# Kernel optimization log

Hardware: AMD Instinct MI355X
Metric: run time of the kernel (lower is better)

The kernel has to match this reference:

```python
import jax, jax.numpy as jnp
import numpy as np
from jax import lax

S, T, B = 32, 32, 512          # src len, tgt len, batch
H, E, A = 1024, 256, 1024      # hidden, embed, attention dim
VS, VT = 64, 70                # source / target char vocab
START = 1                      # data.tar_l2i[start_token]


def _gru_cell(gi, h, W_hh, b_hh):
    """torch GRUCell math. gi = x @ W_ih.T + b_ih, shape (B, 3H)."""
    gh = h @ W_hh.T + b_hh
    ir, iz, in_ = jnp.split(gi, 3, axis=-1)
    hr, hz, hn = jnp.split(gh, 3, axis=-1)
    r = jax.nn.sigmoid(ir + hr)
    z = jax.nn.sigmoid(iz + hz)
    n = jnp.tanh(in_ + r * hn)
    return (1.0 - z) * n + z * h


def setup_inputs() -> dict:
    key = jax.random.key(0)
    ks = jax.random.split(key, 16)
    n = lambda k, shp: jax.random.normal(k, shp, dtype=jnp.float32) * 0.05
    return {
        "source": jax.random.randint(ks[0], (S, B), 0, VS),
        "target": jax.random.randint(ks[1], (T, B), 0, VT),
        "teacher_forcing": 1,
        "emb_src": n(ks[2], (VS, E)),
        "W_ih_enc": n(ks[3], (3 * H, E)),
        "W_hh_enc": n(ks[4], (3 * H, H)),
        "b_ih_enc": n(ks[5], (3 * H,)),
        "b_hh_enc": n(ks[6], (3 * H,)),
        "emb_tgt": n(ks[7], (VT, E)),
        "W_attn": n(ks[8], (2 * H, A)),
        "b_attn": n(ks[9], (A,)),
        "v_attn": n(ks[10], (A,)),
        "W_ih_dec": n(ks[11], (3 * H, H + E)),
        "W_hh_dec": n(ks[12], (3 * H, H)),
        "b_ih_dec": n(ks[13], (3 * H,)),
        "b_hh_dec": n(ks[14], (3 * H,)),
        "W_out": n(ks[15], (H, VT)),
        "b_out": jnp.zeros((VT,), jnp.float32),
    }


def reference(source, target, teacher_forcing, emb_src, W_ih_enc, W_hh_enc,
              b_ih_enc, b_hh_enc, emb_tgt, W_attn, b_attn, v_attn,
              W_ih_dec, W_hh_dec, b_ih_dec, b_hh_dec, W_out, b_out):
    tf = bool(teacher_forcing)

    # ---------------- Encoder: GRU over (S, B) ----------------
    x_emb = emb_src[source]                                   # (S, B, E)
    # precompute input-to-hidden GEMM for all timesteps (big fused GEMM)
    gi_all = jnp.einsum('sbe,ge->sbg', x_emb, W_ih_enc) + b_ih_enc  # (S, B, 3H)

    def enc_step(h, gi_t):
        h = _gru_cell(gi_t, h, W_hh_enc, b_hh_enc)
        return h, h

    h0 = jnp.zeros((B, H), x_emb.dtype)
    h_enc, enc_ops = lax.scan(enc_step, h0, gi_all)           # enc_ops: (S, B, H)

    # ---------------- Decoder loop (t = 1 .. T-1) ----------------
    def dec_step(carry, tgt_t):
        h, x = carry
        emb = emb_tgt[x]                                      # (B, E)
        hx = jnp.broadcast_to(h[None], (S, B, H))
        feat = jnp.concatenate([hx, enc_ops], axis=-1)        # (S, B, 2H)
        energy = jnp.tanh(jnp.einsum('sbf,fa->sba', feat, W_attn) + b_attn)
        scores = energy @ v_attn                              # (S, B)
        alpha = jax.nn.softmax(scores, axis=0)                # over source positions
        ctx = jnp.einsum('sb,sbh->bh', alpha, enc_ops)        # (B, H)
        gi = jnp.concatenate([ctx, emb], axis=-1) @ W_ih_dec.T + b_ih_dec
        h_new = _gru_cell(gi, h, W_hh_dec, b_hh_dec)
        logits = h_new @ W_out + b_out                        # (B, VT)
        x_next = tgt_t if tf else jnp.argmax(logits, axis=1)
        return (h_new, x_next), (logits, alpha.T)             # attn row: (B, S)

    (_, _), (dec_logits, attn) = lax.scan(dec_step, (h_enc, target[0]), target[1:])

    # outputs[0] is the one-hot start token (outputs[:, :, start]=1, rows 1.. overwritten)
    row0 = jnp.zeros((B, VT), dec_logits.dtype).at[:, START].set(1.0)
    outputs = jnp.concatenate([row0[None], dec_logits], axis=0)  # (T, B, VT)
    return outputs, attn                                         # attn: (T-1, B, S)
```

## Files before the change

### kernel.cpp

```cpp
#include <hip/hip_runtime.h>
#include <hip/hip_bf16.h>

typedef __bf16 bfx8 __attribute__((ext_vector_type(8)));
typedef __bf16 bfx4 __attribute__((ext_vector_type(4)));
typedef float f32x4 __attribute__((ext_vector_type(4)));

#define MFMA __builtin_amdgcn_mfma_f32_16x16x32_bf16


__device__ __attribute__((aligned(256))) float  g_h[512 * 1024];
__device__ __attribute__((aligned(256))) float  g_hpart[512 * 1024];
__device__ __attribute__((aligned(256))) __bf16 g_hb[2][512 * 1024];
__device__ __attribute__((aligned(256))) __bf16 g_Adec[512 * 1280];
__device__ __attribute__((aligned(256))) __bf16 g_enc_ops[(size_t)32 * 512 * 1024];
__device__ __attribute__((aligned(256))) __bf16 g_enc_part[(size_t)32 * 512 * 1024];
__device__ __attribute__((aligned(256))) __bf16 g_sWhhe[(size_t)3072 * 1024];
__device__ __attribute__((aligned(256))) __bf16 g_sWihe[(size_t)3072 * 256];
__device__ __attribute__((aligned(256))) __bf16 g_sWhhd[(size_t)3072 * 1024];
__device__ __attribute__((aligned(256))) __bf16 g_sWihd[(size_t)3072 * 1280];
__device__ __attribute__((aligned(256))) __bf16 g_sWattnA[(size_t)1024 * 1024];
__device__ __attribute__((aligned(256))) __bf16 g_sWattnB[(size_t)1024 * 1024];
__device__ __attribute__((aligned(256))) __bf16 g_sWout[(size_t)128 * 1024];
__device__ __attribute__((aligned(256))) __bf16 g_embs[64 * 256];
__device__ __attribute__((aligned(256))) __bf16 g_embt[70 * 256];

__device__ __forceinline__ float fast_tanh(float x) {
    float cx = fminf(fmaxf(x, -15.f), 15.f);
    float e = __expf(-2.f * cx);
    return (1.f - e) / (1.f + e);
}

__global__ void k_cvt(const float* __restrict__ src, __bf16* __restrict__ dst,
                      int n4)
{
    int i = blockIdx.x * 256 + threadIdx.x;
    if (i >= n4) return;
    float4 v = ((const float4*)src)[i];
    __bf16 o[4] = {(__bf16)v.x, (__bf16)v.y, (__bf16)v.z, (__bf16)v.w};
    *(ushort2*)(dst + 4 * i) = *(ushort2*)o;
    *(ushort2*)(dst + 4 * i + 2) = *(ushort2*)(o + 2);
}

__global__ void swz_rm(const float* __restrict__ W, __bf16* __restrict__ out,
                       int nK, int total)
{
    int gid = blockIdx.x * 256 + threadIdx.x;
    if (gid >= total) return;
    int F = gid >> 6, L = gid & 63;
    int t = F / nK, c = F - t * nK;
    int K = nK * 32;
    const float* s = W + (size_t)(t * 16 + (L & 15)) * K + c * 32 + (L >> 4) * 8;
    __bf16 o[8];
#pragma unroll
    for (int u = 0; u < 8; u++) o[u] = (__bf16)s[u];
    *(uint4*)(out + (size_t)gid * 8) = *(uint4*)o;
}

__global__ void swz_cm(const float* __restrict__ W, __bf16* __restrict__ out,
                       int nK, int ldsrc, int nguard, int total)
{
    int gid = blockIdx.x * 256 + threadIdx.x;
    if (gid >= total) return;
    int F = gid >> 6, L = gid & 63;
    int t = F / nK, c = F - t * nK;
    int n = t * 16 + (L & 15);
    int k = c * 32 + (L >> 4) * 8;
    __bf16 o[8];
#pragma unroll
    for (int u = 0; u < 8; u++)
        o[u] = (n < nguard) ? (__bf16)W[(size_t)(k + u) * ldsrc + n] : (__bf16)0.f;
    *(uint4*)(out + (size_t)gid * 8) = *(uint4*)o;
}

__global__ void k_init(float* __restrict__ out)
{
    int idx = blockIdx.x * 256 + threadIdx.x;
    if (idx < 512 * 1024) { g_h[idx] = 0.f; g_hb[0][idx] = (__bf16)0.f; }
    if (idx < 512 * 70) out[idx] = (idx % 70 == 1) ? 1.f : 0.f;
}

__global__ __launch_bounds__(512, 4) void k_encpart(
    const __bf16* __restrict__ Amat, const __bf16* __restrict__ sW,
    __bf16* __restrict__ Cout)
{
    __shared__ __bf16 sA[2][64 * 256];
    const int tid = threadIdx.x;
    const int w = tid >> 6, lane = tid & 63;
    const int r15 = lane & 15, q = lane >> 4;
    const int sw = (blockIdx.x & 7) * 128 + (blockIdx.x >> 3);
    const int nx = sw & 3;
    const int n0 = nx * 256, m0 = (sw >> 2) * 64;

    int sr[4], sv[4], so[4];
#pragma unroll
    for (int i = 0; i < 4; i++) {
        int lin = tid + i * 512;
        sr[i] = lin >> 5;
        sv[i] = lin & 31;
        so[i] = (sr[i] * 32 + (sv[i] ^ (sr[i] & 7))) * 8;
    }

    uint4 regs[4];
#pragma unroll
    for (int i = 0; i < 4; i++)
        regs[i] = *(const uint4*)(Amat + (size_t)(m0 + sr[i]) * 1024 + sv[i] * 8);
#pragma unroll
    for (int i = 0; i < 4; i++)
        *(uint4*)(&sA[0][so[i]]) = regs[i];
    __syncthreads();

    const int xk = r15 & 7;
    f32x4 acc[2][4];
#pragma unroll
    for (int nn = 0; nn < 2; nn++)
#pragma unroll
        for (int mf = 0; mf < 4; mf++) acc[nn][mf] = (f32x4){0.f, 0.f, 0.f, 0.f};

    const __bf16* wp0 = sW + ((size_t)(nx * 16 + w * 2) * 32) * 512 + lane * 8;
    const __bf16* wp1 = wp0 + 32 * 512;
    const int ar0 = r15 * 256;
    const int ar1 = (16 + r15) * 256;
    const int ar2 = (32 + r15) * 256;
    const int ar3 = (48 + r15) * 256;

    for (int kc = 0; kc < 4; kc++) {
        if (kc < 3) {
#pragma unroll
            for (int i = 0; i < 4; i++)
                regs[i] = *(const uint4*)(Amat + (size_t)(m0 + sr[i]) * 1024 +
                                          (kc + 1) * 256 + sv[i] * 8);
        }
        const __bf16* sAb = sA[kc & 1];
        const __bf16* wq0 = wp0 + kc * 8 * 512;
        const __bf16* wq1 = wp1 + kc * 8 * 512;
#pragma unroll
        for (int c = 0; c < 8; c++) {
            int us = ((c * 4 + q) ^ xk) * 8;
            bfx8 a0 = *(const bfx8*)(sAb + ar0 + us);
            bfx8 a1 = *(const bfx8*)(sAb + ar1 + us);
            bfx8 a2 = *(const bfx8*)(sAb + ar2 + us);
            bfx8 a3 = *(const bfx8*)(sAb + ar3 + us);
            bfx8 w0 = *(const bfx8*)(wq0 + c * 512);
            bfx8 w1 = *(const bfx8*)(wq1 + c * 512);
            acc[0][0] = MFMA(a0, w0, acc[0][0], 0, 0, 0);
            acc[0][1] = MFMA(a1, w0, acc[0][1], 0, 0, 0);
            acc[0][2] = MFMA(a2, w0, acc[0][2], 0, 0, 0);
            acc[0][3] = MFMA(a3, w0, acc[0][3], 0, 0, 0);
            acc[1][0] = MFMA(a0, w1, acc[1][0], 0, 0, 0);
            acc[1][1] = MFMA(a1, w1, acc[1][1], 0, 0, 0);
            acc[1][2] = MFMA(a2, w1, acc[1][2], 0, 0, 0);
            acc[1][3] = MFMA(a3, w1, acc[1][3], 0, 0, 0);
        }
        if (kc < 3) {
#pragma unroll
            for (int i = 0; i < 4; i++)
                *(uint4*)(&sA[(kc + 1) & 1][so[i]]) = regs[i];
            __syncthreads();
        }
    }

    __bf16* sC = sA[0];
#pragma unroll
    for (int nn = 0; nn < 2; nn++) {
        const int cl = (w * 2 + nn) * 16 + r15;
#pragma unroll
        for (int mf = 0; mf < 4; mf++) {
#pragma unroll
            for (int reg = 0; reg < 4; reg++) {
                int row = mf * 16 + q * 4 + reg;
                sC[row * 256 + cl] = (__bf16)acc[nn][mf][reg];
            }
        }
    }
    __syncthreads();
#pragma unroll
    for (int i = 0; i < 4; i++) {
        int lin = tid + i * 512;
        int row = lin >> 5, unit = lin & 31;
        *(uint4*)(Cout + (size_t)(m0 + row) * 1024 + n0 + unit * 8) =
            *(const uint4*)(sC + row * 256 + unit * 8);
    }
}

#define GH_BODY(ACC)                                              \
    {                                                             \
        int us = ((c * 4 + q) ^ xk) * 8;                          \
        bfx8 a0 = *(const bfx8*)(sA1 + br0 + us);                 \
        bfx8 a1 = *(const bfx8*)(sA1 + br1 + us);                 \
        bfx8 w0 = *(const bfx8*)(xp0 + c * 512);                  \
        bfx8 w1 = *(const bfx8*)(xp1 + c * 512);                  \
        bfx8 w2 = *(const bfx8*)(xp2 + c * 512);                  \
        ACC[0][0] = MFMA(a0, w0, ACC[0][0], 0, 0, 0);             \
        ACC[0][1] = MFMA(a1, w0, ACC[0][1], 0, 0, 0);             \
        ACC[1][0] = MFMA(a0, w1, ACC[1][0], 0, 0, 0);             \
        ACC[1][1] = MFMA(a1, w1, ACC[1][1], 0, 0, 0);             \
        ACC[2][0] = MFMA(a0, w2, ACC[2][0], 0, 0, 0);             \
        ACC[2][1] = MFMA(a1, w2, ACC[2][1], 0, 0, 0);             \
    }

#define GI_BODY(ACC)                                              \
    {                                                             \
        bfx8 a0 = *(const bfx8*)(A0 + c * 32);                    \
        bfx8 a1 = *(const bfx8*)(A1 + c * 32);                    \
        bfx8 w0 = *(const bfx8*)(wp0 + c * 512);                  \
        bfx8 w1 = *(const bfx8*)(wp1 + c * 512);                  \
        bfx8 w2 = *(const bfx8*)(wp2 + c * 512);                  \
        ACC[0][0] = MFMA(a0, w0, ACC[0][0], 0, 0, 0);             \
        ACC[0][1] = MFMA(a1, w0, ACC[0][1], 0, 0, 0);             \
        ACC[1][0] = MFMA(a0, w1, ACC[1][0], 0, 0, 0);             \
        ACC[1][1] = MFMA(a1, w1, ACC[1][1], 0, 0, 0);             \
        ACC[2][0] = MFMA(a0, w2, ACC[2][0], 0, 0, 0);             \
        ACC[2][1] = MFMA(a1, w2, ACC[2][1], 0, 0, 0);             \
    }

__global__ __launch_bounds__(256, 2) void gru_step(
    const __bf16* __restrict__ hb_in, __bf16* __restrict__ hb_out,
    const __bf16* __restrict__ sW1, const float* __restrict__ b1,
    const __bf16* __restrict__ sW2, const float* __restrict__ b2,
    int nK2, const int* __restrict__ src_t, int enc_t)
{
    __shared__ __align__(16) unsigned char smem[77824];
    __bf16* sA1 = (__bf16*)smem;
    float*  sGi = (float*)smem;
    float*  sGh = (float*)(smem + 65536);
    const int tid = threadIdx.x;
    const int w = tid >> 6, lane = tid & 63;
    const int r15 = lane & 15, q = lane >> 4;
    const int j0 = blockIdx.x * 32, m0 = blockIdx.y * 32;
    const int jsub = w & 1;

#pragma unroll
    for (int i = 0; i < 16; i++) {
        int lin = tid + i * 256;
        int r = lin >> 7, U = lin & 127;
        uint4 v = *(const uint4*)(hb_in + (size_t)(m0 + r) * 1024 + U * 8);
        *(uint4*)(sA1 + (r * 128 + (U ^ (r & 7))) * 8) = v;
    }
    __syncthreads();

    const size_t tb = (size_t)(blockIdx.x * 2 + jsub);
    const int xk = r15 & 7;
    f32x4 acc[3][2], acc2[3][2];
#pragma unroll
    for (int s = 0; s < 3; s++)
#pragma unroll
        for (int ms = 0; ms < 2; ms++) {
            acc[s][ms]  = (f32x4){0.f, 0.f, 0.f, 0.f};
            acc2[s][ms] = (f32x4){0.f, 0.f, 0.f, 0.f};
        }

    if (w < 2) {
        const __bf16* xp0 = sW1 + (tb * 32) * 512 + lane * 8;
        const __bf16* xp1 = sW1 + ((tb + 64) * 32) * 512 + lane * 8;
        const __bf16* xp2 = sW1 + ((tb + 128) * 32) * 512 + lane * 8;
        const int br0 = r15 * 1024, br1 = (16 + r15) * 1024;
        if (src_t) {
#pragma unroll 4
            for (int c = 0; c < 20; c++) GH_BODY(acc)
        } else {
#pragma unroll 8
            for (int c = 0; c < 32; c++) GH_BODY(acc)
            const __bf16* wp0 = sW2 + (tb * 40) * 512 + lane * 8;
            const __bf16* wp1 = sW2 + ((tb + 64) * 40) * 512 + lane * 8;
            const __bf16* wp2 = sW2 + ((tb + 128) * 40) * 512 + lane * 8;
            const __bf16* A0 = g_Adec + (size_t)(m0 + r15) * 1280 + q * 8;
            const __bf16* A1 = A0 + 16 * 1280;
#pragma unroll
            for (int c = 36; c < 40; c++) GI_BODY(acc2)
        }
    } else {
        if (src_t) {
            int s0 = src_t[m0 + r15];      s0 = (s0 < 0) ? 0 : (s0 > 63 ? 63 : s0);
            int s1 = src_t[m0 + 16 + r15]; s1 = (s1 < 0) ? 0 : (s1 > 63 ? 63 : s1);
            const __bf16* A0 = g_embs + s0 * 256 + q * 8;
            const __bf16* A1 = g_embs + s1 * 256 + q * 8;
            const __bf16* wp0 = sW2 + (tb * 8) * 512 + lane * 8;
            const __bf16* wp1 = sW2 + ((tb + 64) * 8) * 512 + lane * 8;
            const __bf16* wp2 = sW2 + ((tb + 128) * 8) * 512 + lane * 8;
#pragma unroll
            for (int c = 0; c < 8; c++) GI_BODY(acc)
            const __bf16* xp0 = sW1 + (tb * 32) * 512 + lane * 8;
            const __bf16* xp1 = sW1 + ((tb + 64) * 32) * 512 + lane * 8;
            const __bf16* xp2 = sW1 + ((tb + 128) * 32) * 512 + lane * 8;
            const int br0 = r15 * 1024, br1 = (16 + r15) * 1024;
#pragma unroll 4
            for (int c = 20; c < 32; c++) GH_BODY(acc2)
#pragma unroll
            for (int s = 0; s < 3; s++)
#pragma unroll
                for (int ms = 0; ms < 2; ms++)
#pragma unroll
                    for (int reg = 0; reg < 4; reg++)
                        sGh[((s * 2 + jsub) * 32 + ms * 16 + q * 4 + reg) * 16 + r15] =
                            acc2[s][ms][reg];
        } else {
            const __bf16* A0 = g_Adec + (size_t)(m0 + r15) * 1280 + q * 8;
            const __bf16* A1 = A0 + 16 * 1280;
            const __bf16* wp0 = sW2 + (tb * 40) * 512 + lane * 8;
            const __bf16* wp1 = sW2 + ((tb + 64) * 40) * 512 + lane * 8;
            const __bf16* wp2 = sW2 + ((tb + 128) * 40) * 512 + lane * 8;
#pragma unroll 4
            for (int c = 0; c < 36; c++) GI_BODY(acc)
        }
    }
    __syncthreads();
    if (w >= 2) {
#pragma unroll
        for (int s = 0; s < 3; s++)
#pragma unroll
            for (int ms = 0; ms < 2; ms++)
#pragma unroll
                for (int reg = 0; reg < 4; reg++)
                    sGi[((s * 2 + jsub) * 32 + ms * 16 + q * 4 + reg) * 16 + r15] =
                        acc[s][ms][reg];
    }
    __syncthreads();
    if (w < 2) {
        const int jj = j0 + jsub * 16 + r15;
        const float bb1[3] = {b1[jj], b1[1024 + jj], b1[2048 + jj]};
        const float bb2[3] = {b2[jj], b2[1024 + jj], b2[2048 + jj]};
#pragma unroll
        for (int ms = 0; ms < 2; ms++) {
#pragma unroll
            for (int reg = 0; reg < 4; reg++) {
                int bl = ms * 16 + q * 4 + reg;
                int b_ = m0 + bl;
                float gh0 = acc[0][ms][reg] + bb1[0];
                float gh1 = acc[1][ms][reg] + bb1[1];
                float gh2 = acc[2][ms][reg] + bb1[2];
                float gi0 = sGi[((0 * 2 + jsub) * 32 + bl) * 16 + r15] + bb2[0];
                float gi1 = sGi[((1 * 2 + jsub) * 32 + bl) * 16 + r15] + bb2[1];
                float gi2 = sGi[((2 * 2 + jsub) * 32 + bl) * 16 + r15] + bb2[2];
                if (src_t) {
                    gh0 += sGh[((0 * 2 + jsub) * 32 + bl) * 16 + r15];
                    gh1 += sGh[((1 * 2 + jsub) * 32 + bl) * 16 + r15];
                    gh2 += sGh[((2 * 2 + jsub) * 32 + bl) * 16 + r15];
                } else {
                    gi0 += acc2[0][ms][reg];
                    gi1 += acc2[1][ms][reg];
                    gi2 += acc2[2][ms][reg];
                }
                float r = 1.f / (1.f + __expf(-(gi0 + gh0)));
                float z = 1.f / (1.f + __expf(-(gi1 + gh1)));
                float n = fast_tanh(gi2 + r * gh2);
                size_t off = (size_t)b_ * 1024 + jj;
                float hv = (1.f - z) * n + z * g_h[off];
                g_h[off] = hv;
                hb_out[off] = (__bf16)hv;
                if (enc_t >= 0)
                    g_enc_ops[(size_t)enc_t * 524288 + off] = (__bf16)hv;
            }
        }
    }
}

__global__ __launch_bounds__(256) void k_hl(
    const __bf16* __restrict__ src, const float* __restrict__ battn,
    const float* __restrict__ bout, int lrow, float* __restrict__ outp)
{
    __shared__ __bf16 sA[32 * 1024];
    const int tid = threadIdx.x;
    const int w = tid >> 6, lane = tid & 63;
    const int r15 = lane & 15, q = lane >> 4;
    const int bx = blockIdx.x, m0 = blockIdx.y * 32;

#pragma unroll
    for (int i = 0; i < 16; i++) {
        int lin = tid + i * 256;
        int r = lin >> 7, U = lin & 127;
        uint4 v = *(const uint4*)(src + (size_t)(m0 + r) * 1024 + U * 8);
        *(uint4*)(sA + (r * 128 + (U ^ (r & 7))) * 8) = v;
    }
    __syncthreads();

    const __bf16* sW;
    int n;
    if (bx < 16) {
        sW = g_sWattnA;
        n = bx * 64 + w * 16 + r15;
    } else {
        if (lrow < 0) return;
        sW = g_sWout;
        n = (bx - 16) * 64 + w * 16 + r15;
    }
    const size_t tb = (size_t)((bx < 16 ? bx : bx - 16) * 4 + w);
    const __bf16* wp = sW + (tb * 32) * 512 + lane * 8;
    const int xk = r15 & 7;
    const int ar0 = r15 * 1024, ar1 = (16 + r15) * 1024;

    f32x4 acc[2];
    acc[0] = (f32x4){0.f, 0.f, 0.f, 0.f};
    acc[1] = (f32x4){0.f, 0.f, 0.f, 0.f};
#pragma unroll 8
    for (int c = 0; c < 32; c++) {
        int us = ((c * 4 + q) ^ xk) * 8;
        bfx8 a0 = *(const bfx8*)(sA + ar0 + us);
        bfx8 a1 = *(const bfx8*)(sA + ar1 + us);
        bfx8 wv = *(const bfx8*)(wp + c * 512);
        acc[0] = MFMA(a0, wv, acc[0], 0, 0, 0);
        acc[1] = MFMA(a1, wv, acc[1], 0, 0, 0);
    }

    if (bx < 16) {
        float bv = battn[n];
#pragma unroll
        for (int ms = 0; ms < 2; ms++)
#pragma unroll
            for (int reg = 0; reg < 4; reg++)
                g_hpart[(size_t)(m0 + ms * 16 + q * 4 + reg) * 1024 + n] =
                    acc[ms][reg] + bv;
    } else if (n < 70) {
        float bv = bout[n];
#pragma unroll
        for (int ms = 0; ms < 2; ms++)
#pragma unroll
            for (int reg = 0; reg < 4; reg++)
                outp[(size_t)lrow * 35840 +
                     (size_t)(m0 + ms * 16 + q * 4 + reg) * 70 + n] =
                    acc[ms][reg] + bv;
    }
}

__global__ __launch_bounds__(256) void k_attn(
    int j, const int* __restrict__ target, const int* __restrict__ tf,
    const float* __restrict__ v_attn, float* __restrict__ out)
{
    const int b = blockIdx.x, tid = threadIdx.x;
    const int lane = tid & 63, wave = tid >> 6;
    __shared__ float sc[32], sal[32];
    __shared__ int sx;
    if (wave == 0) {
        int xv;
        if (j == 0) xv = target[b];
        else if (*tf) xv = target[j * 512 + b];
        else {
            const float* row = out + (size_t)j * 35840 + b * 70;
            float bv = row[lane]; int bi = lane;
            if (lane < 6) {
                float v2 = row[lane + 64];
                if (v2 > bv) { bv = v2; bi = lane + 64; }
            }
#pragma unroll
            for (int off = 32; off; off >>= 1) {
                float ov = __shfl_down(bv, off);
                int   oi = __shfl_down(bi, off);
                if (ov > bv || (ov == bv && oi < bi)) { bv = ov; bi = oi; }
            }
            xv = bi;
        }
        if (lane == 0) sx = (xv < 0) ? 0 : (xv > 69 ? 69 : xv);
    }
    float hpv[16], vsv[16];
    {
        const float* hp = g_hpart + (size_t)b * 1024;
#pragma unroll
        for (int u = 0; u < 8; u++) {
            hpv[u]     = hp[lane * 8 + u];
            hpv[8 + u] = hp[512 + lane * 8 + u];
            vsv[u]     = v_attn[lane * 8 + u];
            vsv[8 + u] = v_attn[512 + lane * 8 + u];
        }
    }
    __syncthreads();
    g_Adec[(size_t)b * 1280 + 1024 + tid] = g_embt[sx * 256 + tid];
    for (int s = wave * 8; s < wave * 8 + 8; s++) {
        const __bf16* ep = g_enc_part + ((size_t)s * 512 + b) * 1024;
        bfx8 e0 = *(const bfx8*)(ep + lane * 8);
        bfx8 e1 = *(const bfx8*)(ep + 512 + lane * 8);
        float part = 0.f;
#pragma unroll
        for (int u = 0; u < 8; u++) {
            part += vsv[u]     * fast_tanh((float)e0[u] + hpv[u]);
            part += vsv[8 + u] * fast_tanh((float)e1[u] + hpv[8 + u]);
        }
#pragma unroll
        for (int off = 32; off; off >>= 1) part += __shfl_down(part, off);
        if (lane == 0) sc[s] = part;
    }
    __syncthreads();
    float mx = sc[0];
#pragma unroll
    for (int s = 1; s < 32; s++) mx = fmaxf(mx, sc[s]);
    float den = 0.f;
#pragma unroll
    for (int s = 0; s < 32; s++) den += __expf(sc[s] - mx);
    float rden = 1.f / den;
    if (tid < 32) {
        float al = __expf(sc[tid] - mx) * rden;
        sal[tid] = al;
        out[1146880 + (size_t)j * 16384 + b * 32 + tid] = al;
    }
    __syncthreads();
    float c0 = 0, c1 = 0, c2 = 0, c3 = 0;
    const __bf16* eo = g_enc_ops + (size_t)b * 1024 + tid * 4;
#pragma unroll 4
    for (int s = 0; s < 32; s++) {
        bfx4 e = *(const bfx4*)(eo + (size_t)s * 524288);
        float al = sal[s];
        c0 += al * (float)e[0]; c1 += al * (float)e[1];
        c2 += al * (float)e[2]; c3 += al * (float)e[3];
    }
    bfx4 o = {(__bf16)c0, (__bf16)c1, (__bf16)c2, (__bf16)c3};
    *(bfx4*)(&g_Adec[(size_t)b * 1280 + tid * 4]) = o;
}

extern "C" void kernel_launch(void* const* d_in, const int* in_sizes, int n_in,
                              void* d_out, int out_size, void* d_ws, size_t ws_size,
                              hipStream_t stream)
{
    const int*   source   = (const int*)d_in[0];
    const int*   target   = (const int*)d_in[1];
    const int*   tf       = (const int*)d_in[2];
    const float* emb_src  = (const float*)d_in[3];
    const float* W_ih_enc = (const float*)d_in[4];
    const float* W_hh_enc = (const float*)d_in[5];
    const float* b_ih_enc = (const float*)d_in[6];
    const float* b_hh_enc = (const float*)d_in[7];
    const float* emb_tgt  = (const float*)d_in[8];
    const float* W_attn   = (const float*)d_in[9];
    const float* b_attn   = (const float*)d_in[10];
    const float* v_attn   = (const float*)d_in[11];
    const float* W_ih_dec = (const float*)d_in[12];
    const float* W_hh_dec = (const float*)d_in[13];
    const float* b_ih_dec = (const float*)d_in[14];
    const float* b_hh_dec = (const float*)d_in[15];
    const float* W_out    = (const float*)d_in[16];
    const float* b_out    = (const float*)d_in[17];
    float* out = (float*)d_out;

    void *p_hb, *p_sWhhe, *p_sWihe, *p_sWhhd, *p_sWihd, *p_sWattnA, *p_sWattnB,
         *p_sWout, *p_embs, *p_embt, *p_enc_ops, *p_enc_part;
    hipGetSymbolAddress(&p_hb,       HIP_SYMBOL(g_hb));
    hipGetSymbolAddress(&p_sWhhe,    HIP_SYMBOL(g_sWhhe));
    hipGetSymbolAddress(&p_sWihe,    HIP_SYMBOL(g_sWihe));
    hipGetSymbolAddress(&p_sWhhd,    HIP_SYMBOL(g_sWhhd));
    hipGetSymbolAddress(&p_sWihd,    HIP_SYMBOL(g_sWihd));
    hipGetSymbolAddress(&p_sWattnA,  HIP_SYMBOL(g_sWattnA));
    hipGetSymbolAddress(&p_sWattnB,  HIP_SYMBOL(g_sWattnB));
    hipGetSymbolAddress(&p_sWout,    HIP_SYMBOL(g_sWout));
    hipGetSymbolAddress(&p_embs,     HIP_SYMBOL(g_embs));
    hipGetSymbolAddress(&p_embt,     HIP_SYMBOL(g_embt));
    hipGetSymbolAddress(&p_enc_ops,  HIP_SYMBOL(g_enc_ops));
    hipGetSymbolAddress(&p_enc_part, HIP_SYMBOL(g_enc_part));
    __bf16* hb0 = (__bf16*)p_hb;
    __bf16* hb1 = hb0 + 512 * 1024;

    k_cvt<<<16, 256, 0, stream>>>(emb_src, (__bf16*)p_embs, 64 * 256 / 4);
    k_cvt<<<18, 256, 0, stream>>>(emb_tgt, (__bf16*)p_embt, 70 * 256 / 4);
    swz_rm<<<1536, 256, 0, stream>>>(W_hh_enc, (__bf16*)p_sWhhe, 32, 393216);
    swz_rm<<<384,  256, 0, stream>>>(W_ih_enc, (__bf16*)p_sWihe, 8,  98304);
    swz_rm<<<1536, 256, 0, stream>>>(W_hh_dec, (__bf16*)p_sWhhd, 32, 393216);
    swz_rm<<<1920, 256, 0, stream>>>(W_ih_dec, (__bf16*)p_sWihd, 40, 491520);
    swz_cm<<<512,  256, 0, stream>>>(W_attn, (__bf16*)p_sWattnA, 32, 1024, 1024, 131072);
    swz_cm<<<512,  256, 0, stream>>>(W_attn + (size_t)1024 * 1024,
                                     (__bf16*)p_sWattnB, 32, 1024, 1024, 131072);
    swz_cm<<<64,   256, 0, stream>>>(W_out,  (__bf16*)p_sWout,   32, 70,   70,   16384);
    k_init<<<2048, 256, 0, stream>>>(out);

    for (int t = 0; t < 32; t++) {
        __bf16* hin  = (t & 1) ? hb1 : hb0;
        __bf16* hout = (t & 1) ? hb0 : hb1;
        gru_step<<<dim3(32, 16), 256, 0, stream>>>(
            hin, hout, (__bf16*)p_sWhhe, b_hh_enc,
            (__bf16*)p_sWihe, b_ih_enc, 8, source + t * 512, t);
    }

    k_encpart<<<dim3(1024), 512, 0, stream>>>(
        (__bf16*)p_enc_ops, (__bf16*)p_sWattnB, (__bf16*)p_enc_part);

    k_hl<<<dim3(18, 16), 256, 0, stream>>>(hb0, b_attn, b_out, -1, out);

    for (int j = 0; j < 31; j++) {
        __bf16* hin  = (j & 1) ? hb1 : hb0;
        __bf16* hout = (j & 1) ? hb0 : hb1;
        k_attn<<<512, 256, 0, stream>>>(j, target, tf, v_attn, out);
        gru_step<<<dim3(32, 16), 256, 0, stream>>>(
            hin, hout, (__bf16*)p_sWhhd, b_hh_dec,
            (__bf16*)p_sWihd, b_ih_dec, 40, nullptr, -1);
        k_hl<<<dim3(18, 16), 256, 0, stream>>>(hout, b_attn, b_out, j + 1, out);
    }
}
```

Before: 2.289 ms.

## Precompute embedding-projection lookup tables and split GRU step into encoder/decoder kernels

Because the GRU input contribution from the embedding depends only on the token id, the input-to-hidden products for all source and target vocab entries are precomputed once into fp32 tables. Per-step GEMMs then gather rows from these tables instead of multiplying embeddings. The encoder step now spends all four waves on the hidden GEMM, each taking half of K, and the decoder's input GEMM shrinks from K=1280 to the K=1024 context part. This cuts per-step MFMA work and rebalances waves, at the cost of scattered table reads and the g_embt buffer growing so k_tbl can read padded 32-row tiles.

Result: faster. 2.087 ms (-8.8%).

```diff
diff --git a/kernel.cpp b/kernel.cpp
--- a/kernel.cpp
+++ b/kernel.cpp
@@ -11,7 +11,7 @@
 __device__ __attribute__((aligned(256))) float  g_h[512 * 1024];
 __device__ __attribute__((aligned(256))) float  g_hpart[512 * 1024];
 __device__ __attribute__((aligned(256))) __bf16 g_hb[2][512 * 1024];
-__device__ __attribute__((aligned(256))) __bf16 g_Adec[512 * 1280];
+__device__ __attribute__((aligned(256))) __bf16 g_Adec[512 * 1024];
 __device__ __attribute__((aligned(256))) __bf16 g_enc_ops[(size_t)32 * 512 * 1024];
 __device__ __attribute__((aligned(256))) __bf16 g_enc_part[(size_t)32 * 512 * 1024];
 __device__ __attribute__((aligned(256))) __bf16 g_sWhhe[(size_t)3072 * 1024];
@@ -22,7 +22,10 @@
 __device__ __attribute__((aligned(256))) __bf16 g_sWattnB[(size_t)1024 * 1024];
 __device__ __attribute__((aligned(256))) __bf16 g_sWout[(size_t)128 * 1024];
 __device__ __attribute__((aligned(256))) __bf16 g_embs[64 * 256];
-__device__ __attribute__((aligned(256))) __bf16 g_embt[70 * 256];
+__device__ __attribute__((aligned(256))) __bf16 g_embt[96 * 256];
+__device__ __attribute__((aligned(256))) float  g_tblS[64 * 3072];
+__device__ __attribute__((aligned(256))) float  g_tblT[70 * 3072];
+__device__ __attribute__((aligned(256))) int    g_xsel[512];
 
 __device__ __forceinline__ float fast_tanh(float x) {
     float cx = fminf(fmaxf(x, -15.f), 15.f);
@@ -77,6 +80,53 @@
     int idx = blockIdx.x * 256 + threadIdx.x;
     if (idx < 512 * 1024) { g_h[idx] = 0.f; g_hb[0][idx] = (__bf16)0.f; }
     if (idx < 512 * 70) out[idx] = (idx % 70 == 1) ? 1.f : 0.f;
+}
+
+__global__ __launch_bounds__(256) void k_tbl(
+    const __bf16* __restrict__ emb, const __bf16* __restrict__ sW,
+    int nKtot, int cOff, int vguard, float* __restrict__ tbl)
+{
+    __shared__ __bf16 sA[32 * 256];
+    const int tid = threadIdx.x;
+    const int w = tid >> 6, lane = tid & 63;
+    const int r15 = lane & 15, q = lane >> 4;
+    const int bx = blockIdx.x, m0 = blockIdx.y * 32;
+
+#pragma unroll
+    for (int i = 0; i < 4; i++) {
+        int lin = tid + i * 256;
+        int r = lin >> 5, U = lin & 31;
+        uint4 v = *(const uint4*)(emb + (size_t)(m0 + r) * 256 + U * 8);
+        *(uint4*)(sA + (r * 32 + (U ^ (r & 7))) * 8) = v;
+    }
+    __syncthreads();
+
+    const size_t tb = (size_t)(bx * 4 + w);
+    const __bf16* wp = sW + (tb * nKtot + cOff) * 512 + lane * 8;
+    const int xk = r15 & 7;
+    const int ar0 = r15 * 256, ar1 = (16 + r15) * 256;
+
+    f32x4 acc[2];
+    acc[0] = (f32x4){0.f, 0.f, 0.f, 0.f};
+    acc[1] = (f32x4){0.f, 0.f, 0.f, 0.f};
+#pragma unroll
+    for (int c = 0; c < 8; c++) {
+        int us = ((c * 4 + q) ^ xk) * 8;
+        bfx8 a0 = *(const bfx8*)(sA + ar0 + us);
+        bfx8 a1 = *(const bfx8*)(sA + ar1 + us);
+        bfx8 wv = *(const bfx8*)(wp + c * 512);
+        acc[0] = MFMA(a0, wv, acc[0], 0, 0, 0);
+        acc[1] = MFMA(a1, wv, acc[1], 0, 0, 0);
+    }
+    const int n = bx * 64 + w * 16 + r15;
+#pragma unroll
+    for (int ms = 0; ms < 2; ms++)
+#pragma unroll
+        for (int reg = 0; reg < 4; reg++) {
+            int row = m0 + ms * 16 + q * 4 + reg;
+            if (row < vguard)
+                tbl[(size_t)row * 3072 + n] = acc[ms][reg];
+        }
 }
 
 __global__ __launch_bounds__(512, 4) void k_encpart(
@@ -213,15 +263,13 @@
         ACC[2][1] = MFMA(a1, w2, ACC[2][1], 0, 0, 0);             \
     }
 
-__global__ __launch_bounds__(256, 2) void gru_step(
+__global__ __launch_bounds__(256, 2) void gru_enc(
     const __bf16* __restrict__ hb_in, __bf16* __restrict__ hb_out,
-    const __bf16* __restrict__ sW1, const float* __restrict__ b1,
-    const __bf16* __restrict__ sW2, const float* __restrict__ b2,
-    int nK2, const int* __restrict__ src_t, int enc_t)
+    const float* __restrict__ b1, const float* __restrict__ b2,
+    const int* __restrict__ src_t, int enc_t)
 {
     __shared__ __align__(16) unsigned char smem[77824];
     __bf16* sA1 = (__bf16*)smem;
-    float*  sGi = (float*)smem;
     float*  sGh = (float*)(smem + 65536);
     const int tid = threadIdx.x;
     const int w = tid >> 6, lane = tid & 63;
@@ -240,70 +288,20 @@
 
     const size_t tb = (size_t)(blockIdx.x * 2 + jsub);
     const int xk = r15 & 7;
-    f32x4 acc[3][2], acc2[3][2];
+    f32x4 acc[3][2];
 #pragma unroll
     for (int s = 0; s < 3; s++)
 #pragma unroll
-        for (int ms = 0; ms < 2; ms++) {
-            acc[s][ms]  = (f32x4){0.f, 0.f, 0.f, 0.f};
-            acc2[s][ms] = (f32x4){0.f, 0.f, 0.f, 0.f};
-        }
-
-    if (w < 2) {
-        const __bf16* xp0 = sW1 + (tb * 32) * 512 + lane * 8;
-        const __bf16* xp1 = sW1 + ((tb + 64) * 32) * 512 + lane * 8;
-        const __bf16* xp2 = sW1 + ((tb + 128) * 32) * 512 + lane * 8;
-        const int br0 = r15 * 1024, br1 = (16 + r15) * 1024;
-        if (src_t) {
-#pragma unroll 4
-            for (int c = 0; c < 20; c++) GH_BODY(acc)
-        } else {
+        for (int ms = 0; ms < 2; ms++) acc[s][ms] = (f32x4){0.f, 0.f, 0.f, 0.f};
+
+    const __bf16* xp0 = g_sWhhe + (tb * 32) * 512 + lane * 8;
+    const __bf16* xp1 = g_sWhhe + ((tb + 64) * 32) * 512 + lane * 8;
+    const __bf16* xp2 = g_sWhhe + ((tb + 128) * 32) * 512 + lane * 8;
+    const int br0 = r15 * 1024, br1 = (16 + r15) * 1024;
+    const int cbeg = (w < 2) ? 0 : 16;
 #pragma unroll 8
-            for (int c = 0; c < 32; c++) GH_BODY(acc)
-            const __bf16* wp0 = sW2 + (tb * 40) * 512 + lane * 8;
-            const __bf16* wp1 = sW2 + ((tb + 64) * 40) * 512 + lane * 8;
-            const __bf16* wp2 = sW2 + ((tb + 128) * 40) * 512 + lane * 8;
-            const __bf16* A0 = g_Adec + (size_t)(m0 + r15) * 1280 + q * 8;
-            const __bf16* A1 = A0 + 16 * 1280;
-#pragma unroll
-            for (int c = 36; c < 40; c++) GI_BODY(acc2)
-        }
-    } else {
-        if (src_t) {
-            int s0 = src_t[m0 + r15];      s0 = (s0 < 0) ? 0 : (s0 > 63 ? 63 : s0);
-            int s1 = src_t[m0 + 16 + r15]; s1 = (s1 < 0) ? 0 : (s1 > 63 ? 63 : s1);
-            const __bf16* A0 = g_embs + s0 * 256 + q * 8;
-            const __bf16* A1 = g_embs + s1 * 256 + q * 8;
-            const __bf16* wp0 = sW2 + (tb * 8) * 512 + lane * 8;
-            const __bf16* wp1 = sW2 + ((tb + 64) * 8) * 512 + lane * 8;
-            const __bf16* wp2 = sW2 + ((tb + 128) * 8) * 512 + lane * 8;
-#pragma unroll
-            for (int c = 0; c < 8; c++) GI_BODY(acc)
-            const __bf16* xp0 = sW1 + (tb * 32) * 512 + lane * 8;
-            const __bf16* xp1 = sW1 + ((tb + 64) * 32) * 512 + lane * 8;
-            const __bf16* xp2 = sW1 + ((tb + 128) * 32) * 512 + lane * 8;
-            const int br0 = r15 * 1024, br1 = (16 + r15) * 1024;
-#pragma unroll 4
-            for (int c = 20; c < 32; c++) GH_BODY(acc2)
-#pragma unroll
-            for (int s = 0; s < 3; s++)
-#pragma unroll
-                for (int ms = 0; ms < 2; ms++)
-#pragma unroll
-                    for (int reg = 0; reg < 4; reg++)
-                        sGh[((s * 2 + jsub) * 32 + ms * 16 + q * 4 + reg) * 16 + r15] =
-                            acc2[s][ms][reg];
-        } else {
-            const __bf16* A0 = g_Adec + (size_t)(m0 + r15) * 1280 + q * 8;
-            const __bf16* A1 = A0 + 16 * 1280;
-            const __bf16* wp0 = sW2 + (tb * 40) * 512 + lane * 8;
-            const __bf16* wp1 = sW2 + ((tb + 64) * 40) * 512 + lane * 8;
-            const __bf16* wp2 = sW2 + ((tb + 128) * 40) * 512 + lane * 8;
-#pragma unroll 4
-            for (int c = 0; c < 36; c++) GI_BODY(acc)
-        }
-    }
-    __syncthreads();
+    for (int c = cbeg; c < cbeg + 16; c++) GH_BODY(acc)
+
     if (w >= 2) {
 #pragma unroll
         for (int s = 0; s < 3; s++)
@@ -311,7 +309,7 @@
             for (int ms = 0; ms < 2; ms++)
 #pragma unroll
                 for (int reg = 0; reg < 4; reg++)
-                    sGi[((s * 2 + jsub) * 32 + ms * 16 + q * 4 + reg) * 16 + r15] =
+                    sGh[((s * 2 + jsub) * 32 + ms * 16 + q * 4 + reg) * 16 + r15] =
                         acc[s][ms][reg];
     }
     __syncthreads();
@@ -325,21 +323,18 @@
             for (int reg = 0; reg < 4; reg++) {
                 int bl = ms * 16 + q * 4 + reg;
                 int b_ = m0 + bl;
-                float gh0 = acc[0][ms][reg] + bb1[0];
-                float gh1 = acc[1][ms][reg] + bb1[1];
-                float gh2 = acc[2][ms][reg] + bb1[2];
-                float gi0 = sGi[((0 * 2 + jsub) * 32 + bl) * 16 + r15] + bb2[0];
-                float gi1 = sGi[((1 * 2 + jsub) * 32 + bl) * 16 + r15] + bb2[1];
-                float gi2 = sGi[((2 * 2 + jsub) * 32 + bl) * 16 + r15] + bb2[2];
-                if (src_t) {
-                    gh0 += sGh[((0 * 2 + jsub) * 32 + bl) * 16 + r15];
-                    gh1 += sGh[((1 * 2 + jsub) * 32 + bl) * 16 + r15];
-                    gh2 += sGh[((2 * 2 + jsub) * 32 + bl) * 16 + r15];
-                } else {
-                    gi0 += acc2[0][ms][reg];
-                    gi1 += acc2[1][ms][reg];
-                    gi2 += acc2[2][ms][reg];
-                }
+                int xv = src_t[b_];
+                xv = (xv < 0) ? 0 : (xv > 63 ? 63 : xv);
+                const float* tv = g_tblS + (size_t)xv * 3072 + jj;
+                float gh0 = acc[0][ms][reg] + bb1[0] +
+                            sGh[((0 * 2 + jsub) * 32 + bl) * 16 + r15];
+                float gh1 = acc[1][ms][reg] + bb1[1] +
+                            sGh[((1 * 2 + jsub) * 32 + bl) * 16 + r15];
+                float gh2 = acc[2][ms][reg] + bb1[2] +
+                            sGh[((2 * 2 + jsub) * 32 + bl) * 16 + r15];
+                float gi0 = tv[0]    + bb2[0];
+                float gi1 = tv[1024] + bb2[1];
+                float gi2 = tv[2048] + bb2[2];
                 float r = 1.f / (1.f + __expf(-(gi0 + gh0)));
                 float z = 1.f / (1.f + __expf(-(gi1 + gh1)));
                 float n = fast_tanh(gi2 + r * gh2);
@@ -347,8 +342,94 @@
                 float hv = (1.f - z) * n + z * g_h[off];
                 g_h[off] = hv;
                 hb_out[off] = (__bf16)hv;
-                if (enc_t >= 0)
-                    g_enc_ops[(size_t)enc_t * 524288 + off] = (__bf16)hv;
+                g_enc_ops[(size_t)enc_t * 524288 + off] = (__bf16)hv;
+            }
+        }
+    }
+}
+
+__global__ __launch_bounds__(256, 2) void gru_dec(
+    const __bf16* __restrict__ hb_in, __bf16* __restrict__ hb_out,
+    const float* __restrict__ b1, const float* __restrict__ b2)
+{
+    __shared__ __align__(16) unsigned char smem[77824];
+    __bf16* sA1 = (__bf16*)smem;
+    float*  sGi = (float*)(smem + 65536);
+    const int tid = threadIdx.x;
+    const int w = tid >> 6, lane = tid & 63;
+    const int r15 = lane & 15, q = lane >> 4;
+    const int j0 = blockIdx.x * 32, m0 = blockIdx.y * 32;
+    const int jsub = w & 1;
+
+#pragma unroll
+    for (int i = 0; i < 16; i++) {
+        int lin = tid + i * 256;
+        int r = lin >> 7, U = lin & 127;
+        uint4 v = *(const uint4*)(hb_in + (size_t)(m0 + r) * 1024 + U * 8);
+        *(uint4*)(sA1 + (r * 128 + (U ^ (r & 7))) * 8) = v;
+    }
+    __syncthreads();
+
+    const size_t tb = (size_t)(blockIdx.x * 2 + jsub);
+    const int xk = r15 & 7;
+    f32x4 acc[3][2];
+#pragma unroll
+    for (int s = 0; s < 3; s++)
+#pragma unroll
+        for (int ms = 0; ms < 2; ms++) acc[s][ms] = (f32x4){0.f, 0.f, 0.f, 0.f};
+
+    if (w < 2) {
+        const __bf16* xp0 = g_sWhhd + (tb * 32) * 512 + lane * 8;
+        const __bf16* xp1 = g_sWhhd + ((tb + 64) * 32) * 512 + lane * 8;
+        const __bf16* xp2 = g_sWhhd + ((tb + 128) * 32) * 512 + lane * 8;
+        const int br0 = r15 * 1024, br1 = (16 + r15) * 1024;
+#pragma unroll 8
+        for (int c = 0; c < 32; c++) GH_BODY(acc)
+    } else {
+        const __bf16* A0 = g_Adec + (size_t)(m0 + r15) * 1024 + q * 8;
+        const __bf16* A1 = A0 + 16 * 1024;
+        const __bf16* wp0 = g_sWihd + (tb * 40) * 512 + lane * 8;
+        const __bf16* wp1 = g_sWihd + ((tb + 64) * 40) * 512 + lane * 8;
+        const __bf16* wp2 = g_sWihd + ((tb + 128) * 40) * 512 + lane * 8;
+#pragma unroll 8
+        for (int c = 0; c < 32; c++) GI_BODY(acc)
+#pragma unroll
+        for (int s = 0; s < 3; s++)
+#pragma unroll
+            for (int ms = 0; ms < 2; ms++)
+#pragma unroll
+                for (int reg = 0; reg < 4; reg++)
+                    sGi[((s * 2 + jsub) * 32 + ms * 16 + q * 4 + reg) * 16 + r15] =
+                        acc[s][ms][reg];
+    }
+    __syncthreads();
+    if (w < 2) {
+        const int jj = j0 + jsub * 16 + r15;
+        const float bb1[3] = {b1[jj], b1[1024 + jj], b1[2048 + jj]};
+        const float bb2[3] = {b2[jj], b2[1024 + jj], b2[2048 + jj]};
+#pragma unroll
+        for (int ms = 0; ms < 2; ms++) {
+#pragma unroll
+            for (int reg = 0; reg < 4; reg++) {
+                int bl = ms * 16 + q * 4 + reg;
+                int b_ = m0 + bl;
+                const float* tv = g_tblT + (size_t)g_xsel[b_] * 3072 + jj;
+                float gh0 = acc[0][ms][reg] + bb1[0];
+                float gh1 = acc[1][ms][reg] + bb1[1];
+                float gh2 = acc[2][ms][reg] + bb1[2];
+                float gi0 = sGi[((0 * 2 + jsub) * 32 + bl) * 16 + r15] +
+                            tv[0]    + bb2[0];
+                float gi1 = sGi[((1 * 2 + jsub) * 32 + bl) * 16 + r15] +
+                            tv[1024] + bb2[1];
+                float gi2 = sGi[((2 * 2 + jsub) * 32 + bl) * 16 + r15] +
+                            tv[2048] + bb2[2];
+                float r = 1.f / (1.f + __expf(-(gi0 + gh0)));
+                float z = 1.f / (1.f + __expf(-(gi1 + gh1)));
+                float n = fast_tanh(gi2 + r * gh2);
+                size_t off = (size_t)b_ * 1024 + jj;
+                float hv = (1.f - z) * n + z * g_h[off];
+                g_h[off] = hv;
+                hb_out[off] = (__bf16)hv;
             }
         }
     }
@@ -462,7 +543,7 @@
         }
     }
     __syncthreads();
-    g_Adec[(size_t)b * 1280 + 1024 + tid] = g_embt[sx * 256 + tid];
+    if (tid == 0) g_xsel[b] = sx;
     for (int s = wave * 8; s < wave * 8 + 8; s++) {
         const __bf16* ep = g_enc_part + ((size_t)s * 512 + b) * 1024;
         bfx8 e0 = *(const bfx8*)(ep + lane * 8);
@@ -501,7 +582,7 @@
         c2 += al * (float)e[2]; c3 += al * (float)e[3];
     }
     bfx4 o = {(__bf16)c0, (__bf16)c1, (__bf16)c2, (__bf16)c3};
-    *(bfx4*)(&g_Adec[(size_t)b * 1280 + tid * 4]) = o;
+    *(bfx4*)(&g_Adec[(size_t)b * 1024 + tid * 4]) = o;
 }
 
 extern "C" void kernel_launch(void* const* d_in, const int* in_sizes, int n_in,
@@ -529,7 +610,7 @@
     float* out = (float*)d_out;
 
     void *p_hb, *p_sWhhe, *p_sWihe, *p_sWhhd, *p_sWihd, *p_sWattnA, *p_sWattnB,
-         *p_sWout, *p_embs, *p_embt, *p_enc_ops, *p_enc_part;
+         *p_sWout, *p_embs, *p_embt, *p_enc_ops, *p_enc_part, *p_tblS, *p_tblT;
     hipGetSymbolAddress(&p_hb,       HIP_SYMBOL(g_hb));
     hipGetSymbolAddress(&p_sWhhe,    HIP_SYMBOL(g_sWhhe));
     hipGetSymbolAddress(&p_sWihe,    HIP_SYMBOL(g_sWihe));
@@ -542,6 +623,8 @@
     hipGetSymbolAddress(&p_embt,     HIP_SYMBOL(g_embt));
     hipGetSymbolAddress(&p_enc_ops,  HIP_SYMBOL(g_enc_ops));
     hipGetSymbolAddress(&p_enc_part, HIP_SYMBOL(g_enc_part));
+    hipGetSymbolAddress(&p_tblS,     HIP_SYMBOL(g_tblS));
+    hipGetSymbolAddress(&p_tblT,     HIP_SYMBOL(g_tblT));
     __bf16* hb0 = (__bf16*)p_hb;
     __bf16* hb1 = hb0 + 512 * 1024;
 
@@ -555,14 +638,17 @@
     swz_cm<<<512,  256, 0, stream>>>(W_attn + (size_t)1024 * 1024,
                                      (__bf16*)p_sWattnB, 32, 1024, 1024, 131072);
     swz_cm<<<64,   256, 0, stream>>>(W_out,  (__bf16*)p_sWout,   32, 70,   70,   16384);
+    k_tbl<<<dim3(48, 2), 256, 0, stream>>>(
+        (__bf16*)p_embs, (__bf16*)p_sWihe, 8,  0,  64, (float*)p_tblS);
+    k_tbl<<<dim3(48, 3), 256, 0, stream>>>(
+        (__bf16*)p_embt, (__bf16*)p_sWihd, 40, 32, 70, (float*)p_tblT);
     k_init<<<2048, 256, 0, stream>>>(out);
 
     for (int t = 0; t < 32; t++) {
         __bf16* hin  = (t & 1) ? hb1 : hb0;
         __bf16* hout = (t & 1) ? hb0 : hb1;
-        gru_step<<<dim3(32, 16), 256, 0, stream>>>(
-            hin, hout, (__bf16*)p_sWhhe, b_hh_enc,
-            (__bf16*)p_sWihe, b_ih_enc, 8, source + t * 512, t);
+        gru_enc<<<dim3(32, 16), 256, 0, stream>>>(
+            hin, hout, b_hh_enc, b_ih_enc, source + t * 512, t);
     }
 
     k_encpart<<<dim3(1024), 512, 0, stream>>>(
@@ -574,9 +660,7 @@
         __bf16* hin  = (j & 1) ? hb1 : hb0;
         __bf16* hout = (j & 1) ? hb0 : hb1;
         k_attn<<<512, 256, 0, stream>>>(j, target, tf, v_attn, out);
-        gru_step<<<dim3(32, 16), 256, 0, stream>>>(
-            hin, hout, (__bf16*)p_sWhhd, b_hh_dec,
-            (__bf16*)p_sWihd, b_ih_dec, 40, nullptr, -1);
+        gru_dec<<<dim3(32, 16), 256, 0, stream>>>(hin, hout, b_hh_dec, b_ih_dec);
         k_hl<<<dim3(18, 16), 256, 0, stream>>>(hout, b_attn, b_out, j + 1, out);
     }
 }
```
